# Kernel optimization log

Measured on AMD Instinct MI355X. Metric: run time of the kernel, lower is better.

Reference implementation:

```python
import jax, jax.numpy as jnp
import numpy as np

B = 4096
D = 64  # emb_dim, hardcoded in UserEmb/ItemEmb


def setup_inputs() -> dict:
    key = jax.random.key(0)
    ks = jax.random.split(key, 26)
    n = lambda k, shape, s=1.0: jax.random.normal(k, shape, dtype=jnp.float32) * s
    inp = {
        'user_emb': jax.random.randint(ks[0], (B, 4), 0, 6, dtype=jnp.int32),
        'item_emb': jax.random.randint(ks[1], (B, 10242), 0, 2, dtype=jnp.int32),
        'edge_emb': jnp.zeros((B,), dtype=jnp.int32),  # edges_emb has num_embeddings=1
        # UserEmb params
        'gender_tab': n(ks[2], (98, D)),
        'age_tab': n(ks[3], (7, D)),
        'occ_tab': n(ks[4], (21, D)),
        'area_tab': n(ks[5], (3402, D)),
        'user_W': n(ks[6], (4 * D, D), 0.05),  # stored [in,out]
        'user_b': n(ks[7], (D,), 0.05),
        # ItemEmb params
        'rate_tab': n(ks[8], (6, D)),
        'genre_W': n(ks[9], (25, D), 0.05),
        'director_W': n(ks[10], (2186, D), 0.02),
        'actor_W': n(ks[11], (8030, D), 0.01),
        'item_W': n(ks[12], (4 * D, D), 0.05),
        'item_b': n(ks[13], (D,), 0.05),
        # GLNFeat params (torch: randn * 0.5)
        'edges_tab': n(ks[14], (1, D)),
        'uu_w': n(ks[15], (D,), 0.5),
        'ui_w': n(ks[16], (D,), 0.5),
        'iu_w': n(ks[17], (D,), 0.5),
        'ii_w': n(ks[18], (D,), 0.5),
        'edge_W': n(ks[19], (D, D), 0.5),
        'uu_W1': n(ks[20], (D, D), 0.5),
        'ui_W1': n(ks[21], (D, D), 0.5),
        'iu_W1': n(ks[22], (D, D), 0.5),
        'ii_W1': n(ks[23], (D, D), 0.5),
    }
    return inp


def _lrelu(v):
    return jnp.where(v >= 0, v, 0.01 * v)  # nn.LeakyReLU default slope


def reference(user_emb, item_emb, edge_emb, gender_tab, age_tab, occ_tab, area_tab,
              user_W, user_b, rate_tab, genre_W, director_W, actor_W, item_W, item_b,
              edges_tab, uu_w, ui_w, iu_w, ii_w, edge_W, uu_W1, ui_W1, iu_W1, ii_W1):
    a = 0.12
    b = 0.12
    # UserEmb
    u_cat = jnp.concatenate([gender_tab[user_emb[:, 0]], age_tab[user_emb[:, 1]],
                             occ_tab[user_emb[:, 2]], area_tab[user_emb[:, 3]]], axis=1)
    x = (u_cat @ user_W + user_b) * a  # [B, D]
    # ItemEmb: multi-hot fields projected then mean-normalized by count
    genre = item_emb[:, 1:26].astype(jnp.float32)
    director = item_emb[:, 26:2212].astype(jnp.float32)
    actor = item_emb[:, 2212:10242].astype(jnp.float32)
    ge = (genre @ genre_W) / jnp.sum(genre, 1, keepdims=True)
    de = (director @ director_W) / jnp.sum(director, 1, keepdims=True)
    ae = (actor @ actor_W) / jnp.sum(actor, 1, keepdims=True)
    i_cat = jnp.concatenate([rate_tab[item_emb[:, 0]], ge, de, ae], axis=1)
    y = (i_cat @ item_W + item_b) * a  # [B, D]
    edge = edges_tab[edge_emb] * b  # [B, D]

    def outer_mm(u, v, M):
        # stop_gradient(outer(u, v) @ M) == u[:,None] * (v @ M), avoids [B,B]
        return jax.lax.stop_gradient(u[:, None] * (v @ M))

    xe = x * edge
    ye = y * edge
    x_xx = xe @ uu_w      # [B]
    x_xy_x = xe @ ui_w
    x_xy_y = ye @ ui_w
    t1 = outer_mm(x_xx, x_xx, x)
    t2 = outer_mm(x_xy_x, x_xy_y, y)
    x_buy = (_lrelu(t1 @ uu_W1) + _lrelu(t2 @ ui_W1)) / 2
    y_yy = ye @ ii_w
    y_yx_y = ye @ iu_w
    y_yx_x = xe @ iu_w
    t3 = outer_mm(y_yy, y_yy, y)
    t4 = outer_mm(y_yx_y, y_yx_x, x)
    y_buy = (_lrelu(t3 @ ii_W1) + _lrelu(t4 @ iu_W1)) / 2
    new = _lrelu(edge @ edge_W)
    return ((x_buy + x) / 2, (y_buy + y) / 2, (new + edge) / 2)
```

## Files before the change

### kernel.cpp

```cpp
#include <hip/hip_runtime.h>
#include <cstddef>

constexpr int BATCH = 4096;
constexpr int ITEM_COLS = 10242;
constexpr int FBTK = 10304;
constexpr int NPART = 15;

constexpr int R_GENDER = 0;
constexpr int R_AGE    = 98;
constexpr int R_OCC    = 105;
constexpr int R_AREA   = 126;
constexpr int R_RATE   = 3528;
constexpr int R_FU     = 3534;

constexpr size_t OFF_FU  = 0;
constexpr size_t OFF_NEW = OFF_FU + (size_t)R_FU * 64;
constexpr size_t OFF_FBT = OFF_NEW + 64;
constexpr size_t OFF_X   = OFF_FBT + (size_t)64 * FBTK / 2;
constexpr size_t OFF_Y   = OFF_X + (size_t)BATCH * 64;
constexpr size_t OFF_P   = OFF_Y + (size_t)BATCH * 64;
constexpr size_t OFF_C   = OFF_P + (size_t)NPART * BATCH * 64;
constexpr size_t OFF_S   = OFF_C + (size_t)NPART * BATCH;
constexpr size_t OFF_SC  = OFF_S + 4ull * 64;

__device__ const int AST[NPART] = {0, 24, 792, 1560, 2208, 2976, 3744, 4512, 5280, 6048, 6816, 7584, 8352, 9120, 9888};
__device__ const int VS [NPART] = {0, 25, 792, 1560, 2211, 2976, 3744, 4512, 5280, 6048, 6816, 7584, 8352, 9120, 9888};
__device__ const int VE [NPART] = {25, 792, 1560, 2211, 2976, 3744, 4512, 5280, 6048, 6816, 7584, 8352, 9120, 9888, 10241};
__device__ const int PLEN[NPART] = {128, 768, 768, 768, 768, 768, 768, 768, 768, 768, 768, 768, 768, 768, 384};

typedef __attribute__((ext_vector_type(8))) short bf16x8;
typedef __attribute__((ext_vector_type(4))) float f32x4;

__device__ __forceinline__ float lrelu(float v) { return v >= 0.0f ? v : 0.01f * v; }

__device__ __forceinline__ unsigned bf_rne_pair(float lo, float hi) {
    unsigned ul = __builtin_bit_cast(unsigned, lo);
    unsigned uh = __builtin_bit_cast(unsigned, hi);
    ul += 0x7fffu + ((ul >> 16) & 1u);
    uh += 0x7fffu + ((uh >> 16) & 1u);
    return (ul >> 16) | (uh & 0xffff0000u);
}

__global__ __launch_bounds__(256) void k_fuse(
        const float* __restrict__ gender_tab, const float* __restrict__ age_tab,
        const float* __restrict__ occ_tab, const float* __restrict__ area_tab,
        const float* __restrict__ user_W, const float* __restrict__ rate_tab,
        const float* __restrict__ genre_W, const float* __restrict__ director_W,
        const float* __restrict__ actor_W, const float* __restrict__ item_W,
        const float* __restrict__ edges_tab, const float* __restrict__ edge_W,
        float* __restrict__ Fu, float* __restrict__ NEWt, short* __restrict__ Fbt,
        float* __restrict__ S) {
    const int t = threadIdx.x;
    const int bx = blockIdx.x;
    if (bx == 0) S[t] = 0.0f;
    if (bx < 884) {
        int n = t & 63;
        int rb = __builtin_amdgcn_readfirstlane(t >> 6);
        int r = bx * 4 + rb;
        if (r > R_FU) return;
        if (r == R_FU) {
            float acc = 0.0f;
#pragma unroll
            for (int k = 0; k < 64; ++k)
                acc = fmaf(edges_tab[k] * 0.12f, edge_W[k * 64 + n], acc);
            NEWt[n] = lrelu(acc);
            return;
        }
        const float* src;
        const float* W;
        if (r < R_AGE)       { src = gender_tab + (size_t)r * 64;            W = user_W;            }
        else if (r < R_OCC)  { src = age_tab    + (size_t)(r - R_AGE) * 64;  W = user_W + 64 * 64;  }
        else if (r < R_AREA) { src = occ_tab    + (size_t)(r - R_OCC) * 64;  W = user_W + 128 * 64; }
        else if (r < R_RATE) { src = area_tab   + (size_t)(r - R_AREA) * 64; W = user_W + 192 * 64; }
        else                 { src = rate_tab   + (size_t)(r - R_RATE) * 64; W = item_W;            }
        float acc = 0.0f;
#pragma unroll
        for (int k = 0; k < 64; ++k)
            acc = fmaf(src[k], W[k * 64 + n], acc);
        Fu[(size_t)r * 64 + n] = acc;
        return;
    }
    const int KT0 = (bx - 884) * 64;
    const int n = t & 63;
    const int rb = __builtin_amdgcn_readfirstlane(t >> 6);
    __shared__ float T[64 * 65];
    for (int rl = 0; rl < 16; ++rl) {
        int r = rl * 4 + rb;
        int KT = KT0 + r;
        float acc = 0.0f;
        if (KT < 10241) {
            const float* src;
            const float* W;
            if (KT < 25)        { src = genre_W    + (size_t)KT * 64;          W = item_W + 64 * 64;  }
            else if (KT < 2211) { src = director_W + (size_t)(KT - 25) * 64;   W = item_W + 128 * 64; }
            else                { src = actor_W    + (size_t)(KT - 2211) * 64; W = item_W + 192 * 64; }
#pragma unroll
            for (int k = 0; k < 64; ++k)
                acc = fmaf(src[k], W[k * 64 + n], acc);
        }
        T[r * 65 + n] = acc;
    }
    __syncthreads();
    int n2 = t >> 2, sg = t & 3;
    unsigned dw[8];
#pragma unroll
    for (int d = 0; d < 8; ++d)
        dw[d] = bf_rne_pair(T[(sg * 16 + 2 * d) * 65 + n2], T[(sg * 16 + 2 * d + 1) * 65 + n2]);
    uint4* dst = (uint4*)(Fbt + (size_t)n2 * FBTK + KT0 + sg * 16);
    dst[0] = make_uint4(dw[0], dw[1], dw[2], dw[3]);
    dst[1] = make_uint4(dw[4], dw[5], dw[6], dw[7]);
}

__global__ __launch_bounds__(256) void k_item(const int* __restrict__ item,
                                              const short* __restrict__ Fbt,
                                              float* __restrict__ P, float* __restrict__ C) {
    const int part = blockIdx.y;
    const int ast = AST[part], vs = VS[part], ve = VE[part], len = PLEN[part];
    const int m0 = blockIdx.x * 64;
    const int t = threadIdx.x;
    const int lane = t & 63;
    const int w = __builtin_amdgcn_readfirstlane(t >> 6);
    const int q = lane >> 4, r16 = lane & 15;
    const int mw = m0 + w * 16;
    const int* __restrict__ ibase = item + (size_t)mw * ITEM_COLS + 1;

    f32x4 acc[5];
#pragma unroll
    for (int s = 0; s < 5; ++s) acc[s] = (f32x4){0.f, 0.f, 0.f, 0.f};

    const short o = (r16 == 0) ? (short)0x3f80 : (short)0;
    const bf16x8 ones = {o, o, o, o, o, o, o, o};

    for (int kb = 0; kb < len; kb += 128) {
        const int K0 = ast + kb;
        unsigned klo = 0, khi = 0;
#pragma unroll
        for (int it = 0; it < 32; ++it) {
            const int rl = it >> 1, h = it & 1;
            int KT = K0 + h * 64 + lane;
            int KTc = KT > 10240 ? 10240 : KT;
            int v = ibase[(size_t)rl * ITEM_COLS + KTc];
            unsigned long long m = __ballot(v != 0 && KT >= vs && KT < ve);
            klo = (lane == it) ? (unsigned)m : klo;
            khi = (lane == it) ? (unsigned)(m >> 32) : khi;
        }
#pragma unroll
        for (int kt = 0; kt < 4; ++kt) {
            unsigned word = __shfl((kt & 1) ? khi : klo, r16 * 2 + (kt >> 1), 64);
            unsigned byte = (word >> (q * 8)) & 0xffu;
            bf16x8 a;
#pragma unroll
            for (int j = 0; j < 8; ++j)
                a[j] = ((byte >> j) & 1u) ? (short)0x3f80 : (short)0;
            const short* fb = Fbt + K0 + kt * 32 + q * 8;
#pragma unroll
            for (int s = 0; s < 4; ++s) {
                bf16x8 b = *(const bf16x8*)(fb + (size_t)(s * 16 + r16) * FBTK);
                acc[s] = __builtin_amdgcn_mfma_f32_16x16x32_bf16(a, b, acc[s], 0, 0, 0);
            }
            acc[4] = __builtin_amdgcn_mfma_f32_16x16x32_bf16(a, ones, acc[4], 0, 0, 0);
        }
    }
    const size_t pb = (size_t)part * BATCH + mw + q * 4;
#pragma unroll
    for (int reg = 0; reg < 4; ++reg) {
        float* pr = P + (pb + reg) * 64 + r16;
        pr[0] = acc[0][reg];
        pr[16] = acc[1][reg];
        pr[32] = acc[2][reg];
        pr[48] = acc[3][reg];
    }
    if (r16 == 0) {
#pragma unroll
        for (int reg = 0; reg < 4; ++reg)
            C[(size_t)part * BATCH + mw + q * 4 + reg] = acc[4][reg];
    }
}

__device__ __forceinline__ float wred(float v) {
#pragma unroll
    for (int m = 1; m < 64; m <<= 1) v += __shfl_xor(v, m, 64);
    return v;
}

__global__ __launch_bounds__(256) void k_mid(const int* __restrict__ item, const int* __restrict__ edge_emb,
                                             const int* __restrict__ user_emb,
                                             const float* __restrict__ Fu, const float* __restrict__ user_b,
                                             const float* __restrict__ P, const float* __restrict__ C,
                                             const float* __restrict__ item_b, const float* __restrict__ edges_tab,
                                             const float* __restrict__ uu_w, const float* __restrict__ ui_w,
                                             const float* __restrict__ iu_w, const float* __restrict__ ii_w,
                                             float* __restrict__ X, float* __restrict__ Y,
                                             float* __restrict__ SC, float* __restrict__ S) {
    const int t = threadIdx.x;
    const int n = t & 63;
    const int wv = __builtin_amdgcn_readfirstlane(t >> 6);
    const float uuw = uu_w[n], uiw = ui_w[n], iuw = iu_w[n], iiw = ii_w[n];
    const float ib = item_b[n], ub = user_b[n];
    const size_t cs = (size_t)BATCH * 64;
    float s1 = 0.0f, s2 = 0.0f, s3 = 0.0f, s4 = 0.0f;

    for (int i = 0; i < 4; ++i) {
        int b = blockIdx.x * 16 + wv * 4 + i;
        const int* ue = user_emb + (size_t)b * 4;
        float x = (Fu[(size_t)(R_GENDER + ue[0]) * 64 + n]
                 + Fu[(size_t)(R_AGE    + ue[1]) * 64 + n]
                 + Fu[(size_t)(R_OCC    + ue[2]) * 64 + n]
                 + Fu[(size_t)(R_AREA   + ue[3]) * 64 + n] + ub) * 0.12f;
        X[(size_t)b * 64 + n] = x;
        int ri = item[(size_t)b * ITEM_COLS];
        size_t base = (size_t)b * 64 + n;
        float sg = P[base], cg = C[b];
        float sd = 0.0f, cd = 0.0f, sa = 0.0f, ca = 0.0f;
#pragma unroll
        for (int p2 = 1; p2 < 4; ++p2)  { sd += P[base + p2 * cs]; cd += C[p2 * BATCH + b]; }
#pragma unroll
        for (int p2 = 4; p2 < 15; ++p2) { sa += P[base + p2 * cs]; ca += C[p2 * BATCH + b]; }
        float y = (Fu[(size_t)(R_RATE + ri) * 64 + n] + sg / cg + sd / cd + sa / ca + ib) * 0.12f;
        Y[(size_t)b * 64 + n] = y;
        float e = edges_tab[(size_t)edge_emb[b] * 64 + n] * 0.12f;
        float xe = x * e, ye = y * e;
        float r1 = wred(xe * uuw);
        float r2 = wred(xe * uiw);
        float r3 = wred(xe * iuw);
        float r4 = wred(ye * uiw);
        float r5 = wred(ye * iiw);
        float r6 = wred(ye * iuw);
        if (n == 0) {
            SC[b] = r1; SC[BATCH + b] = r2; SC[2 * BATCH + b] = r5; SC[3 * BATCH + b] = r6;
        }
        s1 = fmaf(r1, x, s1);
        s2 = fmaf(r4, y, s2);
        s3 = fmaf(r5, y, s3);
        s4 = fmaf(r3, x, s4);
    }
    __shared__ float sp[4][4][64];
    sp[wv][0][n] = s1; sp[wv][1][n] = s2; sp[wv][2][n] = s3; sp[wv][3][n] = s4;
    __syncthreads();
    int i2 = t >> 6;
    float v = sp[0][i2][n] + sp[1][i2][n] + sp[2][i2][n] + sp[3][i2][n];
    atomicAdd(&S[i2 * 64 + n], v);
}

__global__ __launch_bounds__(256) void k_out(const float* __restrict__ X, const float* __restrict__ Y,
                                             const float* __restrict__ SC, const float* __restrict__ S,
                                             const float* __restrict__ uu_W1, const float* __restrict__ ui_W1,
                                             const float* __restrict__ iu_W1, const float* __restrict__ ii_W1,
                                             const float* __restrict__ NEWt, const float* __restrict__ edges_tab,
                                             const int* __restrict__ edge_emb, float* __restrict__ out) {
    const int t = threadIdx.x;
    const int n = t & 63, i = t >> 6;
    __shared__ float sS[4][64], sPB[4][64];
    sS[i][n] = S[i * 64 + n];
    __syncthreads();
    const float* W1 = (i == 0) ? uu_W1 : (i == 1) ? ui_W1 : (i == 2) ? ii_W1 : iu_W1;
    float p = 0.0f;
#pragma unroll
    for (int k = 0; k < 64; ++k) p = fmaf(sS[i][k], W1[k * 64 + n], p);
    sPB[i][n] = p;
    __syncthreads();
    const float p1 = sPB[0][n], p2 = sPB[1][n], p3 = sPB[2][n], p4 = sPB[3][n];
    const float nw = NEWt[n];
    for (int ii = 0; ii < 4; ++ii) {
        int b = blockIdx.x * 16 + i * 4 + ii;
        float xx = SC[b], xyx = SC[BATCH + b], yy = SC[2 * BATCH + b], yxy = SC[3 * BATCH + b];
        float x = X[(size_t)b * 64 + n], y = Y[(size_t)b * 64 + n];
        float o1 = ((lrelu(xx * p1) + lrelu(xyx * p2)) * 0.5f + x) * 0.5f;
        float o2 = ((lrelu(yy * p3) + lrelu(yxy * p4)) * 0.5f + y) * 0.5f;
        float e = edges_tab[(size_t)edge_emb[b] * 64 + n] * 0.12f;
        float o3 = (nw + e) * 0.5f;
        out[(size_t)b * 64 + n] = o1;
        out[((size_t)BATCH + b) * 64 + n] = o2;
        out[((size_t)2 * BATCH + b) * 64 + n] = o3;
    }
}

extern "C" void kernel_launch(void* const* d_in, const int* in_sizes, int n_in,
                              void* d_out, int out_size, void* d_ws, size_t ws_size,
                              hipStream_t stream) {
    (void)in_sizes; (void)n_in; (void)out_size; (void)ws_size;
    const int*   user_emb   = (const int*)  d_in[0];
    const int*   item_emb   = (const int*)  d_in[1];
    const int*   edge_emb   = (const int*)  d_in[2];
    const float* gender_tab = (const float*)d_in[3];
    const float* age_tab    = (const float*)d_in[4];
    const float* occ_tab    = (const float*)d_in[5];
    const float* area_tab   = (const float*)d_in[6];
    const float* user_W     = (const float*)d_in[7];
    const float* user_b     = (const float*)d_in[8];
    const float* rate_tab   = (const float*)d_in[9];
    const float* genre_W    = (const float*)d_in[10];
    const float* director_W = (const float*)d_in[11];
    const float* actor_W    = (const float*)d_in[12];
    const float* item_W     = (const float*)d_in[13];
    const float* item_b     = (const float*)d_in[14];
    const float* edges_tab  = (const float*)d_in[15];
    const float* uu_w       = (const float*)d_in[16];
    const float* ui_w       = (const float*)d_in[17];
    const float* iu_w       = (const float*)d_in[18];
    const float* ii_w       = (const float*)d_in[19];
    const float* edge_W     = (const float*)d_in[20];
    const float* uu_W1      = (const float*)d_in[21];
    const float* ui_W1      = (const float*)d_in[22];
    const float* iu_W1      = (const float*)d_in[23];
    const float* ii_W1      = (const float*)d_in[24];

    float* ws   = (float*)d_ws;
    float* Fu   = ws + OFF_FU;
    float* NEWt = ws + OFF_NEW;
    short* Fbt  = (short*)(ws + OFF_FBT);
    float* X    = ws + OFF_X;
    float* Y    = ws + OFF_Y;
    float* P    = ws + OFF_P;
    float* C    = ws + OFF_C;
    float* S    = ws + OFF_S;
    float* SC   = ws + OFF_SC;
    float* out  = (float*)d_out;

    hipLaunchKernelGGL(k_fuse, dim3(884 + FBTK / 64), dim3(256), 0, stream,
                       gender_tab, age_tab, occ_tab, area_tab, user_W, rate_tab,
                       genre_W, director_W, actor_W, item_W, edges_tab, edge_W, Fu, NEWt, Fbt, S);
    hipLaunchKernelGGL(k_item, dim3(BATCH / 64, NPART), dim3(256), 0, stream, item_emb, Fbt, P, C);
    hipLaunchKernelGGL(k_mid, dim3(BATCH / 16), dim3(256), 0, stream,
                       item_emb, edge_emb, user_emb, Fu, user_b, P, C, item_b, edges_tab,
                       uu_w, ui_w, iu_w, ii_w, X, Y, SC, S);
    hipLaunchKernelGGL(k_out, dim3(BATCH / 16), dim3(256), 0, stream,
                       X, Y, SC, S, uu_W1, ui_W1, iu_W1, ii_W1, NEWt, edges_tab, edge_emb, out);
}
```

Before: 361.7 us.

## Pre-pack item multi-hot bits and tile-swizzle fused weights for MFMA

Adds a separate k_pack kernel that reads each item row once, coalesced, and compresses it into bitmasks per 128-column tile. The fused bf16 weight table is rewritten in a per-tile layout that matches the MFMA operand order, so k_item loads contiguous B fragments instead of strided rows. k_item no longer reads the 168 MB int matrix or shuffles ballots, and it uses templated unrolled tile loops with launch_bounds occupancy 4. The cost is an extra kernel launch and pass over the input, plus scattered stores in k_fuse.

```diff
diff --git a/kernel.cpp b/kernel.cpp
--- a/kernel.cpp
+++ b/kernel.cpp
@@ -3,8 +3,9 @@
 
 constexpr int BATCH = 4096;
 constexpr int ITEM_COLS = 10242;
-constexpr int FBTK = 10304;
 constexpr int NPART = 15;
+constexpr int NTILE = 82;
+constexpr int PK2_DW = NTILE * 4;
 
 constexpr int R_GENDER = 0;
 constexpr int R_AGE    = 98;
@@ -15,30 +16,35 @@
 
 constexpr size_t OFF_FU  = 0;
 constexpr size_t OFF_NEW = OFF_FU + (size_t)R_FU * 64;
-constexpr size_t OFF_FBT = OFF_NEW + 64;
-constexpr size_t OFF_X   = OFF_FBT + (size_t)64 * FBTK / 2;
+constexpr size_t OFF_F3  = OFF_NEW + 64;
+constexpr size_t OFF_PK2 = OFF_F3 + (size_t)NTILE * 8192 / 2;
+constexpr size_t OFF_RI  = OFF_PK2 + (size_t)BATCH * PK2_DW;
+constexpr size_t OFF_X   = OFF_RI + BATCH;
 constexpr size_t OFF_Y   = OFF_X + (size_t)BATCH * 64;
 constexpr size_t OFF_P   = OFF_Y + (size_t)BATCH * 64;
 constexpr size_t OFF_C   = OFF_P + (size_t)NPART * BATCH * 64;
 constexpr size_t OFF_S   = OFF_C + (size_t)NPART * BATCH;
 constexpr size_t OFF_SC  = OFF_S + 4ull * 64;
 
-__device__ const int AST[NPART] = {0, 24, 792, 1560, 2208, 2976, 3744, 4512, 5280, 6048, 6816, 7584, 8352, 9120, 9888};
-__device__ const int VS [NPART] = {0, 25, 792, 1560, 2211, 2976, 3744, 4512, 5280, 6048, 6816, 7584, 8352, 9120, 9888};
-__device__ const int VE [NPART] = {25, 792, 1560, 2211, 2976, 3744, 4512, 5280, 6048, 6816, 7584, 8352, 9120, 9888, 10241};
-__device__ const int PLEN[NPART] = {128, 768, 768, 768, 768, 768, 768, 768, 768, 768, 768, 768, 768, 768, 384};
+__device__ const int AST[NPART]   = {0, 24, 792, 1560, 2208, 2976, 3744, 4512, 5280, 6048, 6816, 7584, 8352, 9120, 9888};
+__device__ const int VS [NPART]   = {0, 25, 792, 1560, 2211, 2976, 3744, 4512, 5280, 6048, 6816, 7584, 8352, 9120, 9888};
+__device__ const int VE [NPART]   = {25, 792, 1560, 2211, 2976, 3744, 4512, 5280, 6048, 6816, 7584, 8352, 9120, 9888, 10241};
+__device__ const int PLEN[NPART]  = {128, 768, 768, 768, 768, 768, 768, 768, 768, 768, 768, 768, 768, 768, 384};
+__device__ const int TBASE[NPART] = {0, 1, 7, 13, 19, 25, 31, 37, 43, 49, 55, 61, 67, 73, 79};
+__device__ const signed char TG2P[NTILE] = {
+    0, 1,1,1,1,1,1, 2,2,2,2,2,2, 3,3,3,3,3,3, 4,4,4,4,4,4, 5,5,5,5,5,5,
+    6,6,6,6,6,6, 7,7,7,7,7,7, 8,8,8,8,8,8, 9,9,9,9,9,9, 10,10,10,10,10,10,
+    11,11,11,11,11,11, 12,12,12,12,12,12, 13,13,13,13,13,13, 14,14,14};
 
 typedef __attribute__((ext_vector_type(8))) short bf16x8;
 typedef __attribute__((ext_vector_type(4))) float f32x4;
 
 __device__ __forceinline__ float lrelu(float v) { return v >= 0.0f ? v : 0.01f * v; }
 
-__device__ __forceinline__ unsigned bf_rne_pair(float lo, float hi) {
-    unsigned ul = __builtin_bit_cast(unsigned, lo);
-    unsigned uh = __builtin_bit_cast(unsigned, hi);
-    ul += 0x7fffu + ((ul >> 16) & 1u);
-    uh += 0x7fffu + ((uh >> 16) & 1u);
-    return (ul >> 16) | (uh & 0xffff0000u);
+__device__ __forceinline__ short bf_rne(float f) {
+    unsigned u = __builtin_bit_cast(unsigned, f);
+    u += 0x7fffu + ((u >> 16) & 1u);
+    return (short)(u >> 16);
 }
 
 __global__ __launch_bounds__(256) void k_fuse(
@@ -48,7 +54,7 @@
         const float* __restrict__ genre_W, const float* __restrict__ director_W,
         const float* __restrict__ actor_W, const float* __restrict__ item_W,
         const float* __restrict__ edges_tab, const float* __restrict__ edge_W,
-        float* __restrict__ Fu, float* __restrict__ NEWt, short* __restrict__ Fbt,
+        float* __restrict__ Fu, float* __restrict__ NEWt, short* __restrict__ F3,
         float* __restrict__ S) {
     const int t = threadIdx.x;
     const int bx = blockIdx.x;
@@ -82,10 +88,10 @@
     }
     const int KT0 = (bx - 884) * 64;
     const int n = t & 63;
-    const int rb = __builtin_amdgcn_readfirstlane(t >> 6);
+    const int g = __builtin_amdgcn_readfirstlane(t >> 6);
     __shared__ float T[64 * 65];
     for (int rl = 0; rl < 16; ++rl) {
-        int r = rl * 4 + rb;
+        int r = rl * 4 + g;
         int KT = KT0 + r;
         float acc = 0.0f;
         if (KT < 10241) {
@@ -101,66 +107,105 @@
         T[r * 65 + n] = acc;
     }
     __syncthreads();
-    int n2 = t >> 2, sg = t & 3;
-    unsigned dw[8];
-#pragma unroll
-    for (int d = 0; d < 8; ++d)
-        dw[d] = bf_rne_pair(T[(sg * 16 + 2 * d) * 65 + n2], T[(sg * 16 + 2 * d + 1) * 65 + n2]);
-    uint4* dst = (uint4*)(Fbt + (size_t)n2 * FBTK + KT0 + sg * 16);
-    dst[0] = make_uint4(dw[0], dw[1], dw[2], dw[3]);
-    dst[1] = make_uint4(dw[4], dw[5], dw[6], dw[7]);
-}
-
-__global__ __launch_bounds__(256) void k_item(const int* __restrict__ item,
-                                              const short* __restrict__ Fbt,
-                                              float* __restrict__ P, float* __restrict__ C) {
+    const int s = n >> 4, r16 = n & 15;
+    for (int rl = 0; rl < 16; ++rl) {
+        int r = rl * 4 + g;
+        int KT = KT0 + r;
+        short v = bf_rne(T[r * 65 + n]);
+        for (int p = 0; p < NPART; ++p) {
+            int d = KT - AST[p];
+            if (d >= 0 && d < PLEN[p]) {
+                int tg = TBASE[p] + (d >> 7);
+                int off = d & 127;
+                int kt = off >> 5, qq = (off >> 3) & 3, j = off & 7;
+                F3[(size_t)tg * 8192 + kt * 2048 + s * 512 + (qq * 16 + r16) * 8 + j] = v;
+            }
+        }
+    }
+}
+
+__global__ __launch_bounds__(256) void k_pack(const int* __restrict__ item,
+                                              unsigned* __restrict__ pk2, int* __restrict__ RI) {
+    const int row = blockIdx.x;
+    const int t = threadIdx.x;
+    const int lane = t & 63;
+    const int w = __builtin_amdgcn_readfirstlane(t >> 6);
+    const int* __restrict__ arow = item + (size_t)row * ITEM_COLS + 1;
+    if (t == 0) RI[row] = item[(size_t)row * ITEM_COLS];
+    for (int tg = w; tg < NTILE; tg += 4) {
+        const int p = TG2P[tg];
+        const int kst = AST[p] + (tg - TBASE[p]) * 128;
+        const int vs = VS[p], ve = VE[p];
+        unsigned dw[4];
+#pragma unroll
+        for (int h = 0; h < 2; ++h) {
+            int KT = kst + h * 64 + lane;
+            int KTc = KT > 10240 ? 10240 : KT;
+            int v = arow[KTc];
+            unsigned long long m = __ballot(v != 0 && KT >= vs && KT < ve);
+            dw[h * 2] = (unsigned)m;
+            dw[h * 2 + 1] = (unsigned)(m >> 32);
+        }
+        if (lane < 4) {
+            unsigned val = (lane & 2) ? ((lane & 1) ? dw[3] : dw[2])
+                                      : ((lane & 1) ? dw[1] : dw[0]);
+            pk2[(size_t)row * PK2_DW + tg * 4 + lane] = val;
+        }
+    }
+}
+
+template <int NT>
+__device__ __forceinline__ void item_body(const uint4* __restrict__ pk2row, int TB,
+                                          const short* __restrict__ F3, int q, int r16,
+                                          f32x4* acc, bf16x8 ones) {
+    uint4 ab[NT];
+#pragma unroll
+    for (int i = 0; i < NT; ++i) ab[i] = pk2row[TB + i];
+#pragma unroll
+    for (int i = 0; i < NT; ++i) {
+        const short* f3t = F3 + (size_t)(TB + i) * 8192 + (q * 16 + r16) * 8;
+        unsigned dws[4] = {ab[i].x, ab[i].y, ab[i].z, ab[i].w};
+#pragma unroll
+        for (int kt = 0; kt < 4; ++kt) {
+            unsigned byte = (dws[kt] >> (q * 8)) & 0xffu;
+            bf16x8 a;
+#pragma unroll
+            for (int j = 0; j < 8; ++j)
+                a[j] = ((byte >> j) & 1u) ? (short)0x3f80 : (short)0;
+#pragma unroll
+            for (int s = 0; s < 4; ++s) {
+                bf16x8 b = *(const bf16x8*)(f3t + kt * 2048 + s * 512);
+                acc[s] = __builtin_amdgcn_mfma_f32_16x16x32_bf16(a, b, acc[s], 0, 0, 0);
+            }
+            acc[4] = __builtin_amdgcn_mfma_f32_16x16x32_bf16(a, ones, acc[4], 0, 0, 0);
+        }
+    }
+}
+
+__global__ __launch_bounds__(256, 4) void k_item(const unsigned* __restrict__ pk2,
+                                                 const short* __restrict__ F3,
+                                                 float* __restrict__ P, float* __restrict__ C) {
     const int part = blockIdx.y;
-    const int ast = AST[part], vs = VS[part], ve = VE[part], len = PLEN[part];
+    const int TB = TBASE[part];
+    const int ntile = PLEN[part] >> 7;
     const int m0 = blockIdx.x * 64;
     const int t = threadIdx.x;
     const int lane = t & 63;
     const int w = __builtin_amdgcn_readfirstlane(t >> 6);
     const int q = lane >> 4, r16 = lane & 15;
     const int mw = m0 + w * 16;
-    const int* __restrict__ ibase = item + (size_t)mw * ITEM_COLS + 1;
+    const uint4* pk2row = (const uint4*)(pk2 + (size_t)(mw + r16) * PK2_DW);
 
     f32x4 acc[5];
 #pragma unroll
     for (int s = 0; s < 5; ++s) acc[s] = (f32x4){0.f, 0.f, 0.f, 0.f};
-
     const short o = (r16 == 0) ? (short)0x3f80 : (short)0;
     const bf16x8 ones = {o, o, o, o, o, o, o, o};
 
-    for (int kb = 0; kb < len; kb += 128) {
-        const int K0 = ast + kb;
-        unsigned klo = 0, khi = 0;
-#pragma unroll
-        for (int it = 0; it < 32; ++it) {
-            const int rl = it >> 1, h = it & 1;
-            int KT = K0 + h * 64 + lane;
-            int KTc = KT > 10240 ? 10240 : KT;
-            int v = ibase[(size_t)rl * ITEM_COLS + KTc];
-            unsigned long long m = __ballot(v != 0 && KT >= vs && KT < ve);
-            klo = (lane == it) ? (unsigned)m : klo;
-            khi = (lane == it) ? (unsigned)(m >> 32) : khi;
-        }
-#pragma unroll
-        for (int kt = 0; kt < 4; ++kt) {
-            unsigned word = __shfl((kt & 1) ? khi : klo, r16 * 2 + (kt >> 1), 64);
-            unsigned byte = (word >> (q * 8)) & 0xffu;
-            bf16x8 a;
-#pragma unroll
-            for (int j = 0; j < 8; ++j)
-                a[j] = ((byte >> j) & 1u) ? (short)0x3f80 : (short)0;
-            const short* fb = Fbt + K0 + kt * 32 + q * 8;
-#pragma unroll
-            for (int s = 0; s < 4; ++s) {
-                bf16x8 b = *(const bf16x8*)(fb + (size_t)(s * 16 + r16) * FBTK);
-                acc[s] = __builtin_amdgcn_mfma_f32_16x16x32_bf16(a, b, acc[s], 0, 0, 0);
-            }
-            acc[4] = __builtin_amdgcn_mfma_f32_16x16x32_bf16(a, ones, acc[4], 0, 0, 0);
-        }
-    }
+    if (ntile == 6)      item_body<6>(pk2row, TB, F3, q, r16, acc, ones);
+    else if (ntile == 3) item_body<3>(pk2row, TB, F3, q, r16, acc, ones);
+    else                 item_body<1>(pk2row, TB, F3, q, r16, acc, ones);
+
     const size_t pb = (size_t)part * BATCH + mw + q * 4;
 #pragma unroll
     for (int reg = 0; reg < 4; ++reg) {
@@ -183,7 +228,7 @@
     return v;
 }
 
-__global__ __launch_bounds__(256) void k_mid(const int* __restrict__ item, const int* __restrict__ edge_emb,
+__global__ __launch_bounds__(256) void k_mid(const int* __restrict__ RI, const int* __restrict__ edge_emb,
                                              const int* __restrict__ user_emb,
                                              const float* __restrict__ Fu, const float* __restrict__ user_b,
                                              const float* __restrict__ P, const float* __restrict__ C,
@@ -208,7 +253,7 @@
                  + Fu[(size_t)(R_OCC    + ue[2]) * 64 + n]
                  + Fu[(size_t)(R_AREA   + ue[3]) * 64 + n] + ub) * 0.12f;
         X[(size_t)b * 64 + n] = x;
-        int ri = item[(size_t)b * ITEM_COLS];
+        int ri = RI[b];
         size_t base = (size_t)b * 64 + n;
         float sg = P[base], cg = C[b];
         float sd = 0.0f, cd = 0.0f, sa = 0.0f, ca = 0.0f;
@@ -305,24 +350,27 @@
     const float* iu_W1      = (const float*)d_in[23];
     const float* ii_W1      = (const float*)d_in[24];
 
-    float* ws   = (float*)d_ws;
-    float* Fu   = ws + OFF_FU;
-    float* NEWt = ws + OFF_NEW;
-    short* Fbt  = (short*)(ws + OFF_FBT);
-    float* X    = ws + OFF_X;
-    float* Y    = ws + OFF_Y;
-    float* P    = ws + OFF_P;
-    float* C    = ws + OFF_C;
-    float* S    = ws + OFF_S;
-    float* SC   = ws + OFF_SC;
-    float* out  = (float*)d_out;
-
-    hipLaunchKernelGGL(k_fuse, dim3(884 + FBTK / 64), dim3(256), 0, stream,
+    float* ws    = (float*)d_ws;
+    float* Fu    = ws + OFF_FU;
+    float* NEWt  = ws + OFF_NEW;
+    short* F3    = (short*)(ws + OFF_F3);
+    unsigned* PK2 = (unsigned*)(ws + OFF_PK2);
+    int*   RI    = (int*)(ws + OFF_RI);
+    float* X     = ws + OFF_X;
+    float* Y     = ws + OFF_Y;
+    float* P     = ws + OFF_P;
+    float* C     = ws + OFF_C;
+    float* S     = ws + OFF_S;
+    float* SC    = ws + OFF_SC;
+    float* out   = (float*)d_out;
+
+    hipLaunchKernelGGL(k_fuse, dim3(1045), dim3(256), 0, stream,
                        gender_tab, age_tab, occ_tab, area_tab, user_W, rate_tab,
-                       genre_W, director_W, actor_W, item_W, edges_tab, edge_W, Fu, NEWt, Fbt, S);
-    hipLaunchKernelGGL(k_item, dim3(BATCH / 64, NPART), dim3(256), 0, stream, item_emb, Fbt, P, C);
+                       genre_W, director_W, actor_W, item_W, edges_tab, edge_W, Fu, NEWt, F3, S);
+    hipLaunchKernelGGL(k_pack, dim3(BATCH), dim3(256), 0, stream, item_emb, PK2, RI);
+    hipLaunchKernelGGL(k_item, dim3(BATCH / 64, NPART), dim3(256), 0, stream, PK2, F3, P, C);
     hipLaunchKernelGGL(k_mid, dim3(BATCH / 16), dim3(256), 0, stream,
-                       item_emb, edge_emb, user_emb, Fu, user_b, P, C, item_b, edges_tab,
+                       RI, edge_emb, user_emb, Fu, user_b, P, C, item_b, edges_tab,
                        uu_w, ui_w, iu_w, ii_w, X, Y, SC, S);
     hipLaunchKernelGGL(k_out, dim3(BATCH / 16), dim3(256), 0, stream,
                        X, Y, SC, S, uu_W1, ui_W1, iu_W1, ii_W1, NEWt, edges_tab, edge_emb, out);
```

Result: no change. 362.6 us (+0.2%).
